# Performance work log

Hardware: AMD Instinct MI355X
Metric: run time of the kernel (lower is better)

## Reference

```python
import jax, jax.numpy as jnp
import numpy as np

B, H, L, DIM = 4, 8, 1024, 256
D = DIM // H  # per-head dim
DEPTH, LAYER_I = 12, 1  # layer_index < depth//4 -> adjacency masking active


def _gcn(xh, adj, W):
    # One graph-convolution layer (GCN used as q/k/v projection in the repo):
    # support = x @ W per head, then aggregate with the (attention-)adjacency.
    # xh: [b,h,t,d], adj: [b,h,l,t], W: [d,d] -> [b,h,l,d]
    return jnp.einsum('bhlt,bhtd->bhld', adj, xh @ W)


def _split_heads(x):
    # 'b t (h d) -> b h t d'
    b, t, _ = x.shape
    return x.reshape(b, t, H, D).transpose(0, 2, 1, 3)


def _merge_heads(v):
    # 'b h t d -> b t (h d)'
    b, h, t, d = v.shape
    return v.transpose(0, 2, 1, 3).reshape(b, t, h * d)


def setup_inputs() -> dict:
    key = jax.random.key(0)
    ks = jax.random.split(key, 9)
    x = jax.random.normal(ks[0], (B, L, DIM), jnp.float32)
    resize_x = jax.random.normal(ks[1], (B, L, DIM), jnpp := jnp.float32) if False else jax.random.normal(ks[1], (B, L, DIM), jnp.float32)
    eye = jnp.eye(L, dtype=jnp.float32)[None, None]  # self-loops so no all-masked rows
    adj = jnp.clip((jax.random.uniform(ks[2], (B, H, L, L)) < 0.1).astype(jnp.float32) + eye, 0.0, 1.0)
    adj_resize = jnp.clip((jax.random.uniform(ks[3], (B, H, L, L)) < 0.1).astype(jnp.float32) + eye, 0.0, 1.0)
    s = D ** -0.5
    Wq = jax.random.normal(ks[4], (D, D), jnp.float32) * s
    Wk = jax.random.normal(ks[5], (D, D), jnp.float32) * s
    Wv = jax.random.normal(ks[6], (D, D), jnp.float32) * s
    R = jax.random.normal(ks[7], (H, H), jnp.float32)  # 'randomatrix' head-mixing param
    Wp = jax.random.normal(ks[8], (DIM, DIM), jnp.float32) * (DIM ** -0.5)  # proj_v (no bias)
    return {'x': x, 'resize_x': resize_x, 'adj': adj, 'adj_resize': adj_resize,
            'Wq': Wq, 'Wk': Wk, 'Wv': Wv, 'R': R, 'Wp': Wp}


def reference(x, resize_x, adj, adj_resize, Wq, Wk, Wv, R, Wp):
    scale = DIM ** -0.5  # note: torch code scales by dim**-0.5 (full dim, not d_head)
    xh = _split_heads(x)          # [b,h,l,d]
    rxh = _split_heads(resize_x)  # [b,h,t,d]
    q = _gcn(xh, adj, Wq)         # [b,h,l,d]
    k = _gcn(rxh, adj_resize, Wk)  # [b,h,t,d]
    attn = jnp.einsum('bhld,bhtd->bhlt', q, k) * scale
    attn = jax.nn.leaky_relu(attn, negative_slope=0.01)
    # cross-head mixing with learned HxH matrix: out[b,i] = sum_h R[i,h]*attn[b,h]
    attn = jnp.einsum('ih,bhlt->bilt', R, attn)
    if LAYER_I < DEPTH // 4:
        attn = jnp.where(adj > 0, attn, -jnp.inf)
    A = jax.nn.softmax(attn, axis=-1)                      # rep_adj
    Ar = jax.nn.softmax(A.transpose(0, 1, 3, 2), axis=-1)  # dual softmax on transpose
    v = _merge_heads(_gcn(xh, A, Wv))
    out = jax.nn.gelu(v, approximate=False) @ Wp
    vr = _merge_heads(_gcn(rxh, Ar, Wv))
    out_resize = jax.nn.gelu(vr, approximate=False) @ Wp
    return out, out_resize, A, Ar
```

## Files before the change

### kernel.cpp

```cpp
#include <hip/hip_runtime.h>
#include <hip/hip_bf16.h>
#include <math.h>

#define BB 4
#define HH 8
#define LL 1024
#define DD 32
#define DIMM 256

typedef unsigned short u16;
typedef unsigned int u32;
typedef short bf16x8 __attribute__((ext_vector_type(8)));
typedef float f32x4 __attribute__((ext_vector_type(4)));

__device__ __forceinline__ float bu2f(u16 s) {
  union { unsigned int u; float f; } cv; cv.u = ((unsigned int)s) << 16; return cv.f;
}
__device__ __forceinline__ u16 f2bu(float f) {
  union { float f; unsigned int u; } cv; cv.f = f;
  unsigned int u = cv.u;
  u += 0x7FFFu + ((u >> 16) & 1u);
  return (u16)(u >> 16);
}
__device__ __forceinline__ short f2bs(float f) {
  return (short)__bfloat16_as_ushort(__float2bfloat16(f));
}

__global__ __launch_bounds__(256) void k_proj(
    const float* __restrict__ x, const float* __restrict__ rx,
    const float* __restrict__ Wq, const float* __restrict__ Wk, const float* __restrict__ Wv,
    u16* __restrict__ xqT_hi, u16* __restrict__ xqT_lo,
    u16* __restrict__ xkT_hi, u16* __restrict__ xkT_lo,
    u16* __restrict__ xvT_hi, u16* __restrict__ xvrT_hi) {
  __shared__ float wq[32][32], wk[32][32], wv[32][32];
  __shared__ float xs[8][32], rxs[8][32];
  __shared__ float tq_[32][9], tk_[32][9], tv_[32][9], tvr_[32][9];
  int tid = threadIdx.x, bid = blockIdx.x;
  int chunk = bid & 127, h = (bid >> 7) & 7, b = bid >> 10;
  int t0 = chunk << 3;
  for (int i = tid; i < 1024; i += 256) {
    int r = i >> 5, c = i & 31;
    wq[r][c] = Wq[i]; wk[r][c] = Wk[i]; wv[r][c] = Wv[i];
  }
  int d = tid & 31, tl = tid >> 5;
  size_t xoff = ((size_t)b * LL + t0 + tl) * DIMM + h * 32 + d;
  xs[tl][d]  = x[xoff];
  rxs[tl][d] = rx[xoff];
  __syncthreads();
  float aq = 0.f, ak = 0.f, av = 0.f, ar = 0.f;
#pragma unroll
  for (int dp = 0; dp < 32; ++dp) {
    float xv_ = xs[tl][dp], rv_ = rxs[tl][dp];
    aq += xv_ * wq[dp][d];
    ak += rv_ * wk[dp][d];
    av += xv_ * wv[dp][d];
    ar += rv_ * wv[dp][d];
  }
  tq_[d][tl] = aq; tk_[d][tl] = ak; tv_[d][tl] = av; tvr_[d][tl] = ar;
  __syncthreads();
  int d2 = tid >> 3, t2 = tid & 7;
  size_t obase = ((size_t)((b * HH + h) * DD + d2)) * LL + t0 + t2;
  {
    float v = tq_[d2][t2]; u16 hi = f2bu(v);
    xqT_hi[obase] = hi; xqT_lo[obase] = f2bu(v - bu2f(hi));
  }
  {
    float v = tk_[d2][t2]; u16 hi = f2bu(v);
    xkT_hi[obase] = hi; xkT_lo[obase] = f2bu(v - bu2f(hi));
  }
  xvT_hi[obase]  = f2bu(tv_[d2][t2]);
  xvrT_hi[obase] = f2bu(tvr_[d2][t2]);
}

template<int PREC, int OUT_SPLIT, int WRITE_BITS>
__global__ __launch_bounds__(256) void k_wmat2(
    const float* __restrict__ wA, const float* __restrict__ wB,
    const u16* __restrict__ sAh, const u16* __restrict__ sAl,
    const u16* __restrict__ sBh, const u16* __restrict__ sBl,
    float* __restrict__ dA, float* __restrict__ dB,
    u16* __restrict__ dAhi, u16* __restrict__ dAlo,
    u16* __restrict__ dBhi, u16* __restrict__ dBlo,
    u32* __restrict__ bits) {
  int tid = threadIdx.x, bid = blockIdx.x;
  int sel = bid >> 9;
  const float* w  = sel ? wB : wA;
  const u16* sh   = sel ? sBh : sAh;
  const u16* sl   = sel ? sBl : sAl;
  float* dst      = sel ? dB : dA;
  u16* dhi        = sel ? dBhi : dAhi;
  u16* dlo        = sel ? dBlo : dAlo;
  int b2 = bid & 511;
  int lc = b2 & 15, bh = b2 >> 4;
  int wave = tid >> 6, lane = tid & 63;
  int l0 = (lc << 6) + (wave << 4);
  int col = lane & 15, g = lane >> 4;
  const float* wrow = w + ((size_t)bh * LL + l0 + col) * LL + (g << 3);
  const u16* b0h = sh + ((size_t)bh * DD + col) * LL + (g << 3);
  const u16* b1h = b0h + 16 * LL;
  const u16* b0l = PREC == 2 ? sl + ((size_t)bh * DD + col) * LL + (g << 3) : nullptr;
  const u16* b1l = PREC == 2 ? b0l + 16 * LL : nullptr;
  unsigned char* bytep = nullptr;
  if (WRITE_BITS && sel == 0)
    bytep = (unsigned char*)(bits + (size_t)bh * 32 * LL + l0 + col) + g;
  f32x4 acc0 = {0.f, 0.f, 0.f, 0.f}, acc1 = {0.f, 0.f, 0.f, 0.f};
#pragma unroll 4
  for (int t0 = 0; t0 < LL; t0 += 32) {
    f32x4 wa = *(const f32x4*)(wrow + t0);
    f32x4 wb = *(const f32x4*)(wrow + t0 + 4);
    bf16x8 whi;
#pragma unroll
    for (int i = 0; i < 4; ++i) {
      whi[i]     = f2bs(wa[i]);
      whi[i + 4] = f2bs(wb[i]);
    }
    if (WRITE_BITS && sel == 0) {
      unsigned int byte = 0;
#pragma unroll
      for (int i = 0; i < 4; ++i) {
        byte |= (wa[i] > 0.f ? 1u : 0u) << i;
        byte |= (wb[i] > 0.f ? 1u : 0u) << (4 + i);
      }
      bytep[(size_t)(t0 >> 5) * (LL * 4)] = (unsigned char)byte;
    }
    bf16x8 s0h = *(const bf16x8*)(b0h + t0);
    bf16x8 s1h = *(const bf16x8*)(b1h + t0);
    acc0 = __builtin_amdgcn_mfma_f32_16x16x32_bf16(whi, s0h, acc0, 0, 0, 0);
    acc1 = __builtin_amdgcn_mfma_f32_16x16x32_bf16(whi, s1h, acc1, 0, 0, 0);
    if (PREC == 2) {
      bf16x8 s0l = *(const bf16x8*)(b0l + t0);
      bf16x8 s1l = *(const bf16x8*)(b1l + t0);
      acc0 = __builtin_amdgcn_mfma_f32_16x16x32_bf16(whi, s0l, acc0, 0, 0, 0);
      acc1 = __builtin_amdgcn_mfma_f32_16x16x32_bf16(whi, s1l, acc1, 0, 0, 0);
    }
  }
#pragma unroll
  for (int i = 0; i < 4; ++i) {
    size_t o = ((size_t)bh * LL + l0 + (g << 2) + i) * DD;
    if (OUT_SPLIT) {
      float v0 = acc0[i]; u16 h0 = f2bu(v0);
      dhi[o + col] = h0; dlo[o + col] = f2bu(v0 - bu2f(h0));
      float v1 = acc1[i]; u16 h1 = f2bu(v1);
      dhi[o + 16 + col] = h1; dlo[o + 16 + col] = f2bu(v1 - bu2f(h1));
    } else {
      dst[o + col] = acc0[i];
      dst[o + 16 + col] = acc1[i];
    }
  }
}

__global__ __launch_bounds__(256) void k_logits_mfma(
    const u16* __restrict__ qh, const u16* __restrict__ ql,
    const u16* __restrict__ kh, const u16* __restrict__ kl,
    const float* __restrict__ Rm, const u32* __restrict__ bits,
    float* __restrict__ M) {
  __shared__ float Rlds[8][8];
  __shared__ float mtile[4][16 * 17];
  int tid = threadIdx.x, bid = blockIdx.x;
  int lb = bid & 15, tb = (bid >> 4) & 7, b = bid >> 7;
  int wave = tid >> 6, lane = tid & 63;
  int l0 = (lb << 6) + (wave << 4);
  int tbase = tb << 7;
  int idx16 = lane & 15, g = lane >> 4;
  if (tid < 64) Rlds[tid >> 3][tid & 7] = Rm[tid];
  bf16x8 qfh[8], qfl[8];
#pragma unroll
  for (int h = 0; h < 8; ++h) {
    size_t off = ((size_t)(b * HH + h) * LL + l0 + idx16) * DD + (g << 3);
    qfh[h] = *(const bf16x8*)(qh + off);
    qfl[h] = *(const bf16x8*)(ql + off);
  }
  __syncthreads();
  int rr_ = lane >> 2, c0 = (lane & 3) << 2;
  for (int tt = 0; tt < 8; ++tt) {
    int t = tbase + (tt << 4);
    f32x4 S[8];
#pragma unroll
    for (int h = 0; h < 8; ++h) {
      size_t koff = ((size_t)(b * HH + h) * LL + t + idx16) * DD + (g << 3);
      bf16x8 bh_ = *(const bf16x8*)(kh + koff);
      bf16x8 bl_ = *(const bf16x8*)(kl + koff);
      f32x4 s = {0.f, 0.f, 0.f, 0.f};
      s = __builtin_amdgcn_mfma_f32_16x16x32_bf16(qfh[h], bh_, s, 0, 0, 0);
      s = __builtin_amdgcn_mfma_f32_16x16x32_bf16(qfl[h], bh_, s, 0, 0, 0);
      s = __builtin_amdgcn_mfma_f32_16x16x32_bf16(qfh[h], bl_, s, 0, 0, 0);
      S[h] = s;
    }
#pragma unroll
    for (int h = 0; h < 8; ++h)
#pragma unroll
      for (int e = 0; e < 4; ++e) {
        float v = S[h][e] * 0.0625f;
        S[h][e] = (v > 0.f) ? v : 0.01f * v;
      }
    int word = t >> 5;
    int bitpos = ((tt & 1) << 4) + idx16;
#pragma unroll
    for (int i = 0; i < 8; ++i) {
      float rr8[8];
#pragma unroll
      for (int h = 0; h < 8; ++h) rr8[h] = Rlds[i][h];
      const u32* bp = bits + ((size_t)(b * HH + i) * 32 + word) * LL + l0 + (g << 2);
      u32 mw0 = bp[0], mw1 = bp[1], mw2 = bp[2], mw3 = bp[3];
      float m_[4];
#pragma unroll
      for (int e = 0; e < 4; ++e) {
        float acc = 0.f;
#pragma unroll
        for (int h = 0; h < 8; ++h) acc += rr8[h] * S[h][e];
        u32 mw = (e == 0) ? mw0 : (e == 1) ? mw1 : (e == 2) ? mw2 : mw3;
        m_[e] = ((mw >> bitpos) & 1u) ? acc : -INFINITY;
      }
#pragma unroll
      for (int e = 0; e < 4; ++e)
        mtile[wave][((g << 2) + e) * 17 + idx16] = m_[e];
      float4 v4;
      v4.x = mtile[wave][rr_ * 17 + c0 + 0];
      v4.y = mtile[wave][rr_ * 17 + c0 + 1];
      v4.z = mtile[wave][rr_ * 17 + c0 + 2];
      v4.w = mtile[wave][rr_ * 17 + c0 + 3];
      *(float4*)(M + ((size_t)(b * HH + i) * LL + l0 + rr_) * LL + t + c0) = v4;
    }
  }
}

__global__ __launch_bounds__(256) void k_norm2v(
    float* __restrict__ A, const u16* __restrict__ xvT,
    float* __restrict__ colpart, float* __restrict__ vb) {
  __shared__ u16 Ast[32][1032];
  int tid = threadIdx.x, bid = blockIdx.x;
  int ch = bid & 31, bh = bid >> 5;
  int wave = tid >> 6, lane = tid & 63;
  float4 colA[4];
#pragma unroll
  for (int j = 0; j < 4; ++j) colA[j] = make_float4(0.f, 0.f, 0.f, 0.f);
  for (int rr = 0; rr < 8; ++rr) {
    int row = (rr << 2) + wave;
    int l = (ch << 5) + row;
    float4* Ap = (float4*)(A + ((size_t)bh * LL + l) * LL);
    float4 v[4];
#pragma unroll
    for (int j = 0; j < 4; ++j) v[j] = Ap[lane + (j << 6)];
    float mx = -INFINITY;
#pragma unroll
    for (int j = 0; j < 4; ++j)
      mx = fmaxf(mx, fmaxf(fmaxf(v[j].x, v[j].y), fmaxf(v[j].z, v[j].w)));
#pragma unroll
    for (int o = 32; o > 0; o >>= 1) mx = fmaxf(mx, __shfl_xor(mx, o, 64));
    float sm = 0.f;
#pragma unroll
    for (int j = 0; j < 4; ++j) {
      v[j].x = __expf(v[j].x - mx); v[j].y = __expf(v[j].y - mx);
      v[j].z = __expf(v[j].z - mx); v[j].w = __expf(v[j].w - mx);
      sm += v[j].x + v[j].y + v[j].z + v[j].w;
    }
#pragma unroll
    for (int o = 32; o > 0; o >>= 1) sm += __shfl_xor(sm, o, 64);
    float inv = 1.0f / sm;
#pragma unroll
    for (int j = 0; j < 4; ++j) {
      v[j].x *= inv; v[j].y *= inv; v[j].z *= inv; v[j].w *= inv;
      colA[j].x += __expf(v[j].x); colA[j].y += __expf(v[j].y);
      colA[j].z += __expf(v[j].z); colA[j].w += __expf(v[j].w);
      Ap[lane + (j << 6)] = v[j];
      int c4 = (lane + (j << 6)) << 2;
      *(short4*)&Ast[row][c4] =
          make_short4(f2bs(v[j].x), f2bs(v[j].y), f2bs(v[j].z), f2bs(v[j].w));
    }
  }
  __syncthreads();
  int idx16 = lane & 15, g = lane >> 4;
  int Mt = wave >> 1, Nt = wave & 1;
  f32x4 acc = {0.f, 0.f, 0.f, 0.f};
  const u16* bbase = xvT + ((size_t)bh * DD + Nt * 16 + idx16) * LL;
#pragma unroll 4
  for (int kc = 0; kc < 32; ++kc) {
    bf16x8 af = *(const bf16x8*)&Ast[(Mt << 4) + idx16][(kc << 5) + (g << 3)];
    bf16x8 bfr = *(const bf16x8*)(bbase + (kc << 5) + (g << 3));
    acc = __builtin_amdgcn_mfma_f32_16x16x32_bf16(af, bfr, acc, 0, 0, 0);
  }
#pragma unroll
  for (int e = 0; e < 4; ++e)
    vb[((size_t)bh * LL + (ch << 5) + (Mt << 4) + (g << 2) + e) * DD + Nt * 16 + idx16] = acc[e];
  __syncthreads();
  float* cf = (float*)&Ast[0][0];
#pragma unroll
  for (int j = 0; j < 4; ++j)
    *(float4*)&cf[wave * 1024 + (j << 8) + (lane << 2)] = colA[j];
  __syncthreads();
  float4 s = make_float4(0.f, 0.f, 0.f, 0.f);
#pragma unroll
  for (int w = 0; w < 4; ++w) {
    float4 t = *(const float4*)&cf[w * 1024 + (tid << 2)];
    s.x += t.x; s.y += t.y; s.z += t.z; s.w += t.w;
  }
  ((float4*)(colpart + ((size_t)bh * 32 + ch) * LL))[tid] = s;
}

__global__ __launch_bounds__(256) void k_arv(
    const float* __restrict__ A, const float* __restrict__ colpart,
    const u16* __restrict__ xvrT, float* __restrict__ Ar, float* __restrict__ vrb) {
  __shared__ float tile[64][65];
  int tid = threadIdx.x, bid = blockIdx.x;
  int tix = bid & 15, bh = bid >> 4;
  int t0 = tix << 6;
  int c = tid & 63, w4 = tid >> 6;
  int idx16 = c & 15, g = (c >> 4) & 3;
  float cs = 0.f;
  {
    const float* cp = colpart + (size_t)bh * 32 * LL + t0 + c;
#pragma unroll
    for (int chk = 0; chk < 32; ++chk) cs += cp[chk * LL];
  }
  float invc = 1.0f / cs;
  f32x4 acc0 = {0.f, 0.f, 0.f, 0.f}, acc1 = {0.f, 0.f, 0.f, 0.f};
  for (int tiy = 0; tiy < 16; ++tiy) {
    int l0 = tiy << 6;
    const float* Ab = A + ((size_t)bh * LL + l0) * LL + t0;
#pragma unroll
    for (int rr = 0; rr < 16; ++rr) {
      int li = (rr << 2) + w4;
      tile[li][c] = __expf(Ab[(size_t)li * LL + c]) * invc;
    }
    __syncthreads();
    float* Arb = Ar + ((size_t)bh * LL + t0) * LL + l0;
#pragma unroll
    for (int rr = 0; rr < 16; ++rr) {
      int ti = (rr << 2) + w4;
      Arb[(size_t)ti * LL + c] = tile[c][ti];
    }
#pragma unroll
    for (int kc = 0; kc < 2; ++kc) {
      bf16x8 af;
#pragma unroll
      for (int j = 0; j < 8; ++j)
        af[j] = f2bs(tile[(kc << 5) + (g << 3) + j][(w4 << 4) + idx16]);
      const u16* bp = xvrT + ((size_t)bh * DD + idx16) * LL + l0 + (kc << 5) + (g << 3);
      bf16x8 b0 = *(const bf16x8*)bp;
      bf16x8 b1 = *(const bf16x8*)(bp + 16 * LL);
      acc0 = __builtin_amdgcn_mfma_f32_16x16x32_bf16(af, b0, acc0, 0, 0, 0);
      acc1 = __builtin_amdgcn_mfma_f32_16x16x32_bf16(af, b1, acc1, 0, 0, 0);
    }
    __syncthreads();
  }
#pragma unroll
  for (int e = 0; e < 4; ++e) {
    size_t o = ((size_t)bh * LL + t0 + (w4 << 4) + (g << 2) + e) * DD;
    vrb[o + idx16] = acc0[e];
    vrb[o + 16 + idx16] = acc1[e];
  }
}

__global__ __launch_bounds__(256) void k_out2(
    const float* __restrict__ vb, const float* __restrict__ vrb,
    const float* __restrict__ Wp,
    float* __restrict__ out, float* __restrict__ outr) {
  __shared__ float g_s[16 * 256];
  __shared__ float wp_s[32 * 256];
  int tid = threadIdx.x, bid = blockIdx.x;
  int sel = bid >> 8;
  const float* vbuf = sel ? vrb : vb;
  float* o = sel ? outr : out;
  int b2 = bid & 255;
  int lt = b2 & 63, b = b2 >> 6;
  int l0 = lt << 4;
  int h = tid >> 5, dd = tid & 31;
#pragma unroll
  for (int r = 0; r < 16; ++r) {
    float v = vbuf[(((size_t)b * HH + h) * LL + l0 + r) * DD + dd];
    g_s[r * 256 + tid] = 0.5f * v * (1.0f + erff(v * 0.70710678118654752f));
  }
  float acc[16];
#pragma unroll
  for (int r = 0; r < 16; ++r) acc[r] = 0.f;
  for (int jc = 0; jc < 8; ++jc) {
    __syncthreads();
#pragma unroll
    for (int u = 0; u < 8; ++u) {
      int idx = tid + (u << 8);
      int j = idx >> 6, c4 = idx & 63;
      float4 v = *(const float4*)(Wp + (size_t)(jc * 32 + j) * DIMM + (c4 << 2));
      *(float4*)&wp_s[j * 256 + (c4 << 2)] = v;
    }
    __syncthreads();
#pragma unroll
    for (int j = 0; j < 32; ++j) {
      float wv = wp_s[j * 256 + tid];
      int jj = (jc << 5) + j;
#pragma unroll
      for (int r = 0; r < 16; ++r)
        acc[r] += g_s[r * 256 + jj] * wv;
    }
  }
#pragma unroll
  for (int r = 0; r < 16; ++r)
    o[((size_t)b * LL + l0 + r) * DIMM + tid] = acc[r];
}

extern "C" void kernel_launch(void* const* d_in, const int* in_sizes, int n_in,
                              void* d_out, int out_size, void* d_ws, size_t ws_size,
                              hipStream_t stream) {
  const float* x    = (const float*)d_in[0];
  const float* rx   = (const float*)d_in[1];
  const float* adj  = (const float*)d_in[2];
  const float* adjr = (const float*)d_in[3];
  const float* Wq   = (const float*)d_in[4];
  const float* Wk   = (const float*)d_in[5];
  const float* Wv   = (const float*)d_in[6];
  const float* Rm   = (const float*)d_in[7];
  const float* Wp   = (const float*)d_in[8];

  const size_t NE = (size_t)BB * HH * LL * DD;

  float* out  = (float*)d_out;
  float* outr = out + NE;
  float* A    = outr + NE;
  float* Ar   = A + (size_t)BB * HH * LL * LL;

  u16* q_hi   = (u16*)(Ar);
  u16* q_lo   = q_hi + NE;
  u16* k_hi   = q_lo + NE;
  u16* k_lo   = k_hi + NE;
  u16* xqT_hi = k_lo + NE;
  u16* xqT_lo = xqT_hi + NE;
  u16* xkT_hi = xqT_lo + NE;
  u16* xkT_lo = xkT_hi + NE;
  u16* xvT_hi  = (u16*)out;
  u16* xvrT_hi = (u16*)outr;

  float* wsf    = (float*)d_ws;
  float* vb     = wsf;
  float* vrb    = wsf + NE;
  float* colpart = wsf + 2 * NE;
  u32* adjbits  = (u32*)(wsf + 3 * NE);

  k_proj<<<4096, 256, 0, stream>>>(x, rx, Wq, Wk, Wv,
                                   xqT_hi, xqT_lo, xkT_hi, xkT_lo,
                                   xvT_hi, xvrT_hi);
  k_wmat2<2,1,1><<<1024, 256, 0, stream>>>(adj, adjr,
                                           xqT_hi, xqT_lo, xkT_hi, xkT_lo,
                                           nullptr, nullptr,
                                           q_hi, q_lo, k_hi, k_lo, adjbits);
  k_logits_mfma<<<512, 256, 0, stream>>>(q_hi, q_lo, k_hi, k_lo, Rm, adjbits, A);
  k_norm2v<<<1024, 256, 0, stream>>>(A, xvT_hi, colpart, vb);
  k_arv<<<512, 256, 0, stream>>>(A, colpart, xvrT_hi, Ar, vrb);
  k_out2<<<512, 256, 0, stream>>>(vb, vrb, Wp, out, outr);
}
```

Measured before the change: 393.7 us.

## Recompute logits in two passes with online softmax stats, drop fp32 A round-trip

Replaces the logits-write plus separate row-softmax kernel with a two-pass scheme: pass 1 computes masked logits and per-row online max/sum partials, and pass 2 recomputes the logits, normalizes them in registers, and writes A once along with a bf16 copy and column-exp partials. The V aggregation moves to a standalone MFMA kernel that reads the bf16 copy, and the transpose-softmax kernel reads bf16 instead of fp32 A. This removes an fp32 read-modify-write of the large A matrix. The cost is computing the logits twice, and the column sums are now built from bf16-rounded values, which may shift Ar slightly.

Measured after the change: 498.1 us. 1.27x slower.

```diff
diff --git a/kernel.cpp b/kernel.cpp
--- a/kernel.cpp
+++ b/kernel.cpp
@@ -148,13 +148,16 @@
   }
 }
 
-__global__ __launch_bounds__(256) void k_logits_mfma(
+template<int PASS>
+__global__ __launch_bounds__(256) void k_logits2(
     const u16* __restrict__ qh, const u16* __restrict__ ql,
     const u16* __restrict__ kh, const u16* __restrict__ kl,
     const float* __restrict__ Rm, const u32* __restrict__ bits,
-    float* __restrict__ M) {
+    float2* __restrict__ mpart,
+    float* __restrict__ A, u16* __restrict__ Ab, float* __restrict__ colpart2) {
   __shared__ float Rlds[8][8];
   __shared__ float mtile[4][16 * 17];
+  __shared__ float2 mstat[8][64];
   int tid = threadIdx.x, bid = blockIdx.x;
   int lb = bid & 15, tb = (bid >> 4) & 7, b = bid >> 7;
   int wave = tid >> 6, lane = tid & 63;
@@ -162,6 +165,21 @@
   int tbase = tb << 7;
   int idx16 = lane & 15, g = lane >> 4;
   if (tid < 64) Rlds[tid >> 3][tid & 7] = Rm[tid];
+  if (PASS == 2) {
+    for (int idx = tid; idx < 512; idx += 256) {
+      int i = idx >> 6, lr = idx & 63;
+      float2 st = make_float2(-INFINITY, 0.f);
+      const float2* mp = mpart + ((size_t)(b * HH + i) * 8) * LL + (lb << 6) + lr;
+#pragma unroll
+      for (int tb2 = 0; tb2 < 8; ++tb2) {
+        float2 p = mp[(size_t)tb2 * LL];
+        float nm = fmaxf(st.x, p.x);
+        if (nm != -INFINITY)
+          st = make_float2(nm, st.y * __expf(st.x - nm) + p.y * __expf(p.x - nm));
+      }
+      mstat[i][lr] = make_float2(st.x, 1.0f / st.y);
+    }
+  }
   bf16x8 qfh[8], qfl[8];
 #pragma unroll
   for (int h = 0; h < 8; ++h) {
@@ -170,6 +188,18 @@
     qfl[h] = *(const bf16x8*)(ql + off);
   }
   __syncthreads();
+  float omx[8][4], osm[8][4];
+  float pmx[8][4], pin[8][4];
+#pragma unroll
+  for (int i = 0; i < 8; ++i)
+#pragma unroll
+    for (int e = 0; e < 4; ++e) {
+      if (PASS == 1) { omx[i][e] = -INFINITY; osm[i][e] = 0.f; }
+      else {
+        float2 st = mstat[i][(wave << 4) + (g << 2) + e];
+        pmx[i][e] = st.x; pin[i][e] = st.y;
+      }
+    }
   int rr_ = lane >> 2, c0 = (lane & 3) << 2;
   for (int tt = 0; tt < 8; ++tt) {
     int t = tbase + (tt << 4);
@@ -210,94 +240,96 @@
         u32 mw = (e == 0) ? mw0 : (e == 1) ? mw1 : (e == 2) ? mw2 : mw3;
         m_[e] = ((mw >> bitpos) & 1u) ? acc : -INFINITY;
       }
-#pragma unroll
-      for (int e = 0; e < 4; ++e)
-        mtile[wave][((g << 2) + e) * 17 + idx16] = m_[e];
-      float4 v4;
-      v4.x = mtile[wave][rr_ * 17 + c0 + 0];
-      v4.y = mtile[wave][rr_ * 17 + c0 + 1];
-      v4.z = mtile[wave][rr_ * 17 + c0 + 2];
-      v4.w = mtile[wave][rr_ * 17 + c0 + 3];
-      *(float4*)(M + ((size_t)(b * HH + i) * LL + l0 + rr_) * LL + t + c0) = v4;
-    }
-  }
-}
-
-__global__ __launch_bounds__(256) void k_norm2v(
-    float* __restrict__ A, const u16* __restrict__ xvT,
-    float* __restrict__ colpart, float* __restrict__ vb) {
-  __shared__ u16 Ast[32][1032];
-  int tid = threadIdx.x, bid = blockIdx.x;
-  int ch = bid & 31, bh = bid >> 5;
+      if (PASS == 1) {
+#pragma unroll
+        for (int e = 0; e < 4; ++e) {
+          float m = m_[e];
+          if (m > omx[i][e]) {
+            osm[i][e] = osm[i][e] * __expf(omx[i][e] - m) + 1.0f;
+            omx[i][e] = m;
+          } else if (m != -INFINITY) {
+            osm[i][e] += __expf(m - omx[i][e]);
+          }
+        }
+      } else {
+        float a_[4];
+        float cs = 0.f;
+#pragma unroll
+        for (int e = 0; e < 4; ++e) {
+          float a = (m_[e] == -INFINITY) ? 0.f : __expf(m_[e] - pmx[i][e]) * pin[i][e];
+          a_[e] = a;
+          cs += __expf(a);
+        }
+        cs += __shfl_xor(cs, 16);
+        cs += __shfl_xor(cs, 32);
+        if (g == 0)
+          colpart2[((((size_t)(b * HH + i) * 16 + lb) * 4 + wave)) * LL + t + idx16] = cs;
+#pragma unroll
+        for (int e = 0; e < 4; ++e)
+          mtile[wave][((g << 2) + e) * 17 + idx16] = a_[e];
+        float4 v4;
+        v4.x = mtile[wave][rr_ * 17 + c0 + 0];
+        v4.y = mtile[wave][rr_ * 17 + c0 + 1];
+        v4.z = mtile[wave][rr_ * 17 + c0 + 2];
+        v4.w = mtile[wave][rr_ * 17 + c0 + 3];
+        size_t rowoff = ((size_t)(b * HH + i) * LL + l0 + rr_) * LL + t + c0;
+        *(float4*)(A + rowoff) = v4;
+        *(short4*)(Ab + rowoff) =
+            make_short4(f2bs(v4.x), f2bs(v4.y), f2bs(v4.z), f2bs(v4.w));
+      }
+    }
+  }
+  if (PASS == 1) {
+#pragma unroll
+    for (int i = 0; i < 8; ++i)
+#pragma unroll
+      for (int e = 0; e < 4; ++e) {
+        float mx = omx[i][e], sm = osm[i][e];
+#pragma unroll
+        for (int msk = 1; msk <= 8; msk <<= 1) {
+          float mx2 = __shfl_xor(mx, msk);
+          float sm2 = __shfl_xor(sm, msk);
+          float nm = fmaxf(mx, mx2);
+          if (nm == -INFINITY) sm = 0.f;
+          else sm = sm * __expf(mx - nm) + sm2 * __expf(mx2 - nm);
+          mx = nm;
+        }
+        if (idx16 == 0)
+          mpart[((size_t)(b * HH + i) * 8 + tb) * LL + l0 + (g << 2) + e] =
+              make_float2(mx, sm);
+      }
+  }
+}
+
+__global__ __launch_bounds__(256) void k_vb(
+    const u16* __restrict__ Ab, const u16* __restrict__ xvT, float* __restrict__ vb) {
+  int tid = threadIdx.x, bid = blockIdx.x;
+  int lc = bid & 15, bh = bid >> 4;
   int wave = tid >> 6, lane = tid & 63;
-  float4 colA[4];
-#pragma unroll
-  for (int j = 0; j < 4; ++j) colA[j] = make_float4(0.f, 0.f, 0.f, 0.f);
-  for (int rr = 0; rr < 8; ++rr) {
-    int row = (rr << 2) + wave;
-    int l = (ch << 5) + row;
-    float4* Ap = (float4*)(A + ((size_t)bh * LL + l) * LL);
-    float4 v[4];
-#pragma unroll
-    for (int j = 0; j < 4; ++j) v[j] = Ap[lane + (j << 6)];
-    float mx = -INFINITY;
-#pragma unroll
-    for (int j = 0; j < 4; ++j)
-      mx = fmaxf(mx, fmaxf(fmaxf(v[j].x, v[j].y), fmaxf(v[j].z, v[j].w)));
-#pragma unroll
-    for (int o = 32; o > 0; o >>= 1) mx = fmaxf(mx, __shfl_xor(mx, o, 64));
-    float sm = 0.f;
-#pragma unroll
-    for (int j = 0; j < 4; ++j) {
-      v[j].x = __expf(v[j].x - mx); v[j].y = __expf(v[j].y - mx);
-      v[j].z = __expf(v[j].z - mx); v[j].w = __expf(v[j].w - mx);
-      sm += v[j].x + v[j].y + v[j].z + v[j].w;
-    }
-#pragma unroll
-    for (int o = 32; o > 0; o >>= 1) sm += __shfl_xor(sm, o, 64);
-    float inv = 1.0f / sm;
-#pragma unroll
-    for (int j = 0; j < 4; ++j) {
-      v[j].x *= inv; v[j].y *= inv; v[j].z *= inv; v[j].w *= inv;
-      colA[j].x += __expf(v[j].x); colA[j].y += __expf(v[j].y);
-      colA[j].z += __expf(v[j].z); colA[j].w += __expf(v[j].w);
-      Ap[lane + (j << 6)] = v[j];
-      int c4 = (lane + (j << 6)) << 2;
-      *(short4*)&Ast[row][c4] =
-          make_short4(f2bs(v[j].x), f2bs(v[j].y), f2bs(v[j].z), f2bs(v[j].w));
-    }
-  }
-  __syncthreads();
+  int l0 = (lc << 6) + (wave << 4);
   int idx16 = lane & 15, g = lane >> 4;
-  int Mt = wave >> 1, Nt = wave & 1;
-  f32x4 acc = {0.f, 0.f, 0.f, 0.f};
-  const u16* bbase = xvT + ((size_t)bh * DD + Nt * 16 + idx16) * LL;
+  const u16* arow = Ab + ((size_t)bh * LL + l0 + idx16) * LL + (g << 3);
+  const u16* b0 = xvT + ((size_t)bh * DD + idx16) * LL + (g << 3);
+  const u16* b1 = b0 + 16 * LL;
+  f32x4 acc0 = {0.f, 0.f, 0.f, 0.f}, acc1 = {0.f, 0.f, 0.f, 0.f};
 #pragma unroll 4
-  for (int kc = 0; kc < 32; ++kc) {
-    bf16x8 af = *(const bf16x8*)&Ast[(Mt << 4) + idx16][(kc << 5) + (g << 3)];
-    bf16x8 bfr = *(const bf16x8*)(bbase + (kc << 5) + (g << 3));
-    acc = __builtin_amdgcn_mfma_f32_16x16x32_bf16(af, bfr, acc, 0, 0, 0);
-  }
-#pragma unroll
-  for (int e = 0; e < 4; ++e)
-    vb[((size_t)bh * LL + (ch << 5) + (Mt << 4) + (g << 2) + e) * DD + Nt * 16 + idx16] = acc[e];
-  __syncthreads();
-  float* cf = (float*)&Ast[0][0];
-#pragma unroll
-  for (int j = 0; j < 4; ++j)
-    *(float4*)&cf[wave * 1024 + (j << 8) + (lane << 2)] = colA[j];
-  __syncthreads();
-  float4 s = make_float4(0.f, 0.f, 0.f, 0.f);
-#pragma unroll
-  for (int w = 0; w < 4; ++w) {
-    float4 t = *(const float4*)&cf[w * 1024 + (tid << 2)];
-    s.x += t.x; s.y += t.y; s.z += t.z; s.w += t.w;
-  }
-  ((float4*)(colpart + ((size_t)bh * 32 + ch) * LL))[tid] = s;
+  for (int t0 = 0; t0 < LL; t0 += 32) {
+    bf16x8 af = *(const bf16x8*)(arow + t0);
+    bf16x8 bb0 = *(const bf16x8*)(b0 + t0);
+    bf16x8 bb1 = *(const bf16x8*)(b1 + t0);
+    acc0 = __builtin_amdgcn_mfma_f32_16x16x32_bf16(af, bb0, acc0, 0, 0, 0);
+    acc1 = __builtin_amdgcn_mfma_f32_16x16x32_bf16(af, bb1, acc1, 0, 0, 0);
+  }
+#pragma unroll
+  for (int e = 0; e < 4; ++e) {
+    size_t o = ((size_t)bh * LL + l0 + (g << 2) + e) * DD;
+    vb[o + idx16] = acc0[e];
+    vb[o + 16 + idx16] = acc1[e];
+  }
 }
 
 __global__ __launch_bounds__(256) void k_arv(
-    const float* __restrict__ A, const float* __restrict__ colpart,
+    const u16* __restrict__ Ab, const float* __restrict__ colpart2,
     const u16* __restrict__ xvrT, float* __restrict__ Ar, float* __restrict__ vrb) {
   __shared__ float tile[64][65];
   int tid = threadIdx.x, bid = blockIdx.x;
@@ -307,19 +339,19 @@
   int idx16 = c & 15, g = (c >> 4) & 3;
   float cs = 0.f;
   {
-    const float* cp = colpart + (size_t)bh * 32 * LL + t0 + c;
-#pragma unroll
-    for (int chk = 0; chk < 32; ++chk) cs += cp[chk * LL];
+    const float* cp = colpart2 + (size_t)bh * 64 * LL + t0 + c;
+#pragma unroll
+    for (int chk = 0; chk < 64; ++chk) cs += cp[(size_t)chk * LL];
   }
   float invc = 1.0f / cs;
   f32x4 acc0 = {0.f, 0.f, 0.f, 0.f}, acc1 = {0.f, 0.f, 0.f, 0.f};
   for (int tiy = 0; tiy < 16; ++tiy) {
     int l0 = tiy << 6;
-    const float* Ab = A + ((size_t)bh * LL + l0) * LL + t0;
+    const u16* Abp = Ab + ((size_t)bh * LL + l0) * LL + t0;
 #pragma unroll
     for (int rr = 0; rr < 16; ++rr) {
       int li = (rr << 2) + w4;
-      tile[li][c] = __expf(Ab[(size_t)li * LL + c]) * invc;
+      tile[li][c] = __expf(bu2f(Abp[(size_t)li * LL + c])) * invc;
     }
     __syncthreads();
     float* Arb = Ar + ((size_t)bh * LL + t0) * LL + l0;
@@ -427,11 +459,13 @@
   u16* xvT_hi  = (u16*)out;
   u16* xvrT_hi = (u16*)outr;
 
-  float* wsf    = (float*)d_ws;
-  float* vb     = wsf;
-  float* vrb    = wsf + NE;
-  float* colpart = wsf + 2 * NE;
-  u32* adjbits  = (u32*)(wsf + 3 * NE);
+  float* wsf      = (float*)d_ws;
+  float* vb       = wsf;
+  float* vrb      = wsf + NE;
+  float* colpart2 = wsf + 2 * NE;
+  u32* adjbits    = (u32*)(wsf + 4 * NE);
+  float2* mpart   = (float2*)(wsf + 5 * NE);
+  u16* Ab         = (u16*)(wsf + 6 * NE);
 
   k_proj<<<4096, 256, 0, stream>>>(x, rx, Wq, Wk, Wv,
                                    xqT_hi, xqT_lo, xkT_hi, xkT_lo,
@@ -440,8 +474,11 @@
                                            xqT_hi, xqT_lo, xkT_hi, xkT_lo,
                                            nullptr, nullptr,
                                            q_hi, q_lo, k_hi, k_lo, adjbits);
-  k_logits_mfma<<<512, 256, 0, stream>>>(q_hi, q_lo, k_hi, k_lo, Rm, adjbits, A);
-  k_norm2v<<<1024, 256, 0, stream>>>(A, xvT_hi, colpart, vb);
-  k_arv<<<512, 256, 0, stream>>>(A, colpart, xvrT_hi, Ar, vrb);
+  k_logits2<1><<<512, 256, 0, stream>>>(q_hi, q_lo, k_hi, k_lo, Rm, adjbits,
+                                        mpart, nullptr, nullptr, nullptr);
+  k_logits2<2><<<512, 256, 0, stream>>>(q_hi, q_lo, k_hi, k_lo, Rm, adjbits,
+                                        mpart, A, Ab, colpart2);
+  k_vb<<<512, 256, 0, stream>>>(Ab, xvT_hi, vb);
+  k_arv<<<512, 256, 0, stream>>>(Ab, colpart2, xvrT_hi, Ar, vrb);
   k_out2<<<512, 256, 0, stream>>>(vb, vrb, Wp, out, outr);
 }
```
